# Optimization experiments

Hardware: AMD Instinct MI355X
Metric: run time of the kernel (lower is better)

The kernel has to match this reference:

```python
import jax, jax.numpy as jnp
import numpy as np

N_NODES = 100000
N_EDGES = 1600000
VOCAB = 1000
EMB = 128
HID = 256
N_GRAPHS = 128
N_LABELS = 2


def setup_inputs() -> dict:
    key = jax.random.key(0)
    ks = jax.random.split(key, 16)
    s = 0.05
    inp = {
        "x_ids": jax.random.randint(ks[0], (N_NODES,), 0, VOCAB),
        "edge_index": jax.random.randint(ks[1], (2, N_EDGES), 0, N_NODES),
        "batch": jnp.sort(jax.random.randint(ks[2], (N_NODES,), 0, N_GRAPHS)),
        "emb": jax.random.normal(ks[3], (VOCAB, EMB)) * s,
        "W0": jax.random.normal(ks[4], (EMB, HID)) * s,
        "b0": jnp.zeros((HID,)),
        "W1": jax.random.normal(ks[5], (HID, HID)) * s,
        "b1": jnp.zeros((HID,)),
        "W2": jax.random.normal(ks[6], (HID, HID)) * s,
        "b2": jnp.zeros((HID,)),
        "W3": jax.random.normal(ks[7], (HID, HID)) * s,
        "b3": jnp.zeros((HID,)),
        "Wc1": jax.random.normal(ks[8], (2 * HID, HID)) * s,
        "bc1": jnp.zeros((HID,)),
        "Wc2": jax.random.normal(ks[9], (HID, N_LABELS)) * s,
        "bc2": jnp.zeros((N_LABELS,)),
    }
    return inp


def _gcn_conv(x, W, b, src, dst, dis):
    # GCNConv with self-loops: out = D^-1/2 (A+I) D^-1/2 (x W) + b
    xw = x @ W                                   # [N, H]
    norm = dis[src] * dis[dst]                   # [E]
    out = jnp.zeros_like(xw).at[dst].add(xw[src] * norm[:, None])
    out = out + xw * (dis * dis)[:, None]        # self-loop term
    return out + b


def reference(x_ids, edge_index, batch, emb, W0, b0, W1, b1, W2, b2, W3, b3,
              Wc1, bc1, Wc2, bc2):
    src, dst = edge_index[0], edge_index[1]
    # degree (incl. self loop) is the same every layer -> compute once
    deg = jnp.zeros((N_NODES,), jnp.float32).at[dst].add(1.0) + 1.0
    dis = jax.lax.rsqrt(deg)

    x = emb[x_ids]                               # [N, EMB]
    for W, b in ((W0, b0), (W1, b1), (W2, b2), (W3, b3)):
        x = jax.nn.relu(_gcn_conv(x, W, b, src, dst, dis))
        # dropout: identity in eval mode

    counts = jax.ops.segment_sum(jnp.ones((N_NODES,), x.dtype), batch,
                                 num_segments=N_GRAPHS)
    mean_pool = jax.ops.segment_sum(x, batch, num_segments=N_GRAPHS)
    mean_pool = mean_pool / jnp.maximum(counts, 1.0)[:, None]
    max_pool = jax.ops.segment_max(x, batch, num_segments=N_GRAPHS)
    max_pool = jnp.where(counts[:, None] > 0, max_pool, 0.0)

    g = jnp.concatenate([mean_pool, max_pool], axis=1)  # [G, 2H]
    h = jax.nn.relu(g @ Wc1 + bc1)
    logits = h @ Wc2 + bc2                               # [G, 2]
    return logits
```

## Files before the change

### kernel.cpp

```cpp
#include <hip/hip_runtime.h>
#include <hip/hip_bf16.h>
#include <cstdint>
#include <cstddef>

#define N_NODES 100000
#define N_EDGES 1600000
#define EMBD 128
#define HID 256
#define N_GRAPHS 128
#define VOCAB 1000
#define NB_SCAN 98

typedef short bf16x8 __attribute__((ext_vector_type(8)));
typedef float f32x4 __attribute__((ext_vector_type(4)));
typedef float f32x2 __attribute__((ext_vector_type(2)));

__device__ inline unsigned short rne_bf16(float f) {
  unsigned u = __float_as_uint(f);
  return (unsigned short)((u + 0x7FFFu + ((u >> 16) & 1u)) >> 16);
}
__device__ inline float bf16_to_f32(unsigned short h) {
  return __uint_as_float(((unsigned)h) << 16);
}
__device__ inline void split_hl(float v, unsigned short& h, unsigned short& l) {
  h = rne_bf16(v);
  float hf = __uint_as_float(((unsigned)h) << 16);
  l = rne_bf16(v - hf);
}
__device__ inline f32x4 cvt4(uint2 v) {
  f32x4 r;
  r[0] = __uint_as_float(v.x << 16);
  r[1] = __uint_as_float(v.x & 0xFFFF0000u);
  r[2] = __uint_as_float(v.y << 16);
  r[3] = __uint_as_float(v.y & 0xFFFF0000u);
  return r;
}
__device__ inline f32x2 cvt2(unsigned v) {
  f32x2 r;
  r[0] = __uint_as_float(v << 16);
  r[1] = __uint_as_float(v & 0xFFFF0000u);
  return r;
}

__global__ void k_indeg(const int* __restrict__ dst, int* __restrict__ indeg) {
  int e = blockIdx.x * 256 + threadIdx.x;
  if (e < N_EDGES) atomicAdd(&indeg[dst[e]], 1);
}

__global__ __launch_bounds__(1024)
void k_scan1(const int* __restrict__ indeg, int* __restrict__ off, int* __restrict__ bsum,
             float* __restrict__ dis) {
  __shared__ int s[1024];
  const int tid = threadIdx.x;
  int i = blockIdx.x * 1024 + tid;
  int v = (i < N_NODES) ? indeg[i] : 0;
  if (i < N_NODES) dis[i] = rsqrtf((float)(v + 1));
  s[tid] = v; __syncthreads();
  #pragma unroll
  for (int ofs = 1; ofs < 1024; ofs <<= 1) {
    int t2 = (tid >= ofs) ? s[tid - ofs] : 0;
    __syncthreads();
    s[tid] += t2;
    __syncthreads();
  }
  if (i < N_NODES) off[i] = s[tid] - v;
  if (tid == 1023) bsum[blockIdx.x] = s[1023];
}

__global__ void k_scan2(int* __restrict__ bsum) {
  if (threadIdx.x == 0) {
    int a = 0;
    for (int i = 0; i < NB_SCAN; ++i) { int t = bsum[i]; bsum[i] = a; a += t; }
    bsum[NB_SCAN] = a;
  }
}

__global__ __launch_bounds__(1024)
void k_scan3(int* __restrict__ off, int* __restrict__ cur, const int* __restrict__ bsum) {
  int i = blockIdx.x * 1024 + threadIdx.x;
  if (i < N_NODES) { int v = off[i] + bsum[blockIdx.x]; off[i] = v; cur[i] = v; }
  if (i == 0) off[N_NODES] = bsum[NB_SCAN];
}

__global__ void k_fill(const int* __restrict__ src, const int* __restrict__ dst,
                       const int* __restrict__ ids, const float* __restrict__ dis,
                       int* __restrict__ cursor, int2* __restrict__ csre,
                       int2* __restrict__ csre0) {
  int e = blockIdx.x * 256 + threadIdx.x;
  if (e < N_EDGES) {
    int s = src[e];
    float ds = dis[s];
    int p = atomicAdd(&cursor[dst[e]], 1);
    csre[p]  = make_int2(s, __float_as_int(ds));
    csre0[p] = make_int2(ids[s], __float_as_int(ds));
  }
}

__global__ void k_prep(const float* __restrict__ emb, unsigned short* __restrict__ emb16,
                       const float* __restrict__ W0, unsigned short* __restrict__ w0h,
                       unsigned short* __restrict__ w0l,
                       const float* __restrict__ W1, unsigned short* __restrict__ w1h,
                       unsigned short* __restrict__ w1l,
                       const float* __restrict__ W2, unsigned short* __restrict__ w2h,
                       unsigned short* __restrict__ w2l,
                       const float* __restrict__ W3, unsigned short* __restrict__ w3h,
                       unsigned short* __restrict__ w3l) {
  int i = blockIdx.x * 256 + threadIdx.x;
  if (i < VOCAB * EMBD) { emb16[i] = rne_bf16(emb[i]); return; }
  i -= VOCAB * EMBD;
  unsigned short h, l;
  if (i < EMBD * HID) {
    int k = i >> 8, n = i & 255;
    split_hl(W0[i], h, l);
    w0h[n * EMBD + k] = h; w0l[n * EMBD + k] = l;
    return;
  }
  i -= EMBD * HID;
  if (i >= 3 * HID * HID) return;
  int w = i >> 16, j = i & 65535;
  const float* Ws = (w == 0) ? W1 : (w == 1) ? W2 : W3;
  unsigned short* th = (w == 0) ? w1h : (w == 1) ? w2h : w3h;
  unsigned short* tl = (w == 0) ? w1l : (w == 1) ? w2l : w3l;
  int k = j >> 8, n = j & 255;
  split_hl(Ws[j], h, l);
  th[n * HID + k] = h; tl[n * HID + k] = l;
}

__global__ __launch_bounds__(256)
void k_agg0(const unsigned short* __restrict__ emb16, const int* __restrict__ ids,
            const float* __restrict__ dis, const int* __restrict__ off,
            const int2* __restrict__ csre0, unsigned short* __restrict__ aggA) {
  const int lane = threadIdx.x & 63;
  const int node = blockIdx.x * 4 + (threadIdx.x >> 6);
  const float di = dis[node];
  unsigned sv = *((const unsigned*)(emb16 + (size_t)ids[node] * EMBD) + lane);
  f32x2 a0 = di * cvt2(sv);
  f32x2 a1 = (f32x2)0.f, a2 = (f32x2)0.f, a3 = (f32x2)0.f;
  const int e0 = off[node], e1 = off[node + 1];
  int e = e0;
  for (; e + 4 <= e1; e += 4) {
    int2 c0 = csre0[e], c1 = csre0[e + 1], c2 = csre0[e + 2], c3 = csre0[e + 3];
    unsigned v0 = *((const unsigned*)(emb16 + (size_t)c0.x * EMBD) + lane);
    unsigned v1 = *((const unsigned*)(emb16 + (size_t)c1.x * EMBD) + lane);
    unsigned v2 = *((const unsigned*)(emb16 + (size_t)c2.x * EMBD) + lane);
    unsigned v3 = *((const unsigned*)(emb16 + (size_t)c3.x * EMBD) + lane);
    a0 += __int_as_float(c0.y) * cvt2(v0);
    a1 += __int_as_float(c1.y) * cvt2(v1);
    a2 += __int_as_float(c2.y) * cvt2(v2);
    a3 += __int_as_float(c3.y) * cvt2(v3);
  }
  for (; e < e1; ++e) {
    int2 c0 = csre0[e];
    unsigned v0 = *((const unsigned*)(emb16 + (size_t)c0.x * EMBD) + lane);
    a0 += __int_as_float(c0.y) * cvt2(v0);
  }
  f32x2 r = di * ((a0 + a1) + (a2 + a3));
  size_t base = (size_t)node * EMBD + lane * 2;
  *(ushort2*)&aggA[base] = make_ushort2(rne_bf16(r[0]), rne_bf16(r[1]));
}

__global__ __launch_bounds__(256)
void k_agg16(const unsigned short* __restrict__ y16, const float* __restrict__ dis,
             const int* __restrict__ off, const int2* __restrict__ csre,
             unsigned short* __restrict__ aggA) {
  const int lane = threadIdx.x & 63;
  const int node = blockIdx.x * 4 + (threadIdx.x >> 6);
  const float di = dis[node];
  uint2 sv = *((const uint2*)(y16 + (size_t)node * HID) + lane);
  f32x4 a0 = di * cvt4(sv);
  f32x4 a1 = (f32x4)0.f, a2 = (f32x4)0.f, a3 = (f32x4)0.f;
  const int e0 = off[node], e1 = off[node + 1];
  int e = e0;
  for (; e + 4 <= e1; e += 4) {
    int2 c0 = csre[e], c1 = csre[e + 1], c2 = csre[e + 2], c3 = csre[e + 3];
    uint2 v0 = *((const uint2*)(y16 + (size_t)c0.x * HID) + lane);
    uint2 v1 = *((const uint2*)(y16 + (size_t)c1.x * HID) + lane);
    uint2 v2 = *((const uint2*)(y16 + (size_t)c2.x * HID) + lane);
    uint2 v3 = *((const uint2*)(y16 + (size_t)c3.x * HID) + lane);
    a0 += __int_as_float(c0.y) * cvt4(v0);
    a1 += __int_as_float(c1.y) * cvt4(v1);
    a2 += __int_as_float(c2.y) * cvt4(v2);
    a3 += __int_as_float(c3.y) * cvt4(v3);
  }
  for (; e < e1; ++e) {
    int2 c0 = csre[e];
    uint2 v0 = *((const uint2*)(y16 + (size_t)c0.x * HID) + lane);
    a0 += __int_as_float(c0.y) * cvt4(v0);
  }
  f32x4 r = di * ((a0 + a1) + (a2 + a3));
  size_t base = (size_t)node * HID + lane * 4;
  *(ushort4*)&aggA[base] = make_ushort4(rne_bf16(r[0]), rne_bf16(r[1]),
                                        rne_bf16(r[2]), rne_bf16(r[3]));
}

__device__ inline void gl_lds16(const void* g, void* l) {
  __builtin_amdgcn_global_load_lds((const __attribute__((address_space(1))) unsigned int*)g,
                                   (__attribute__((address_space(3))) unsigned int*)l,
                                   16, 0, 0);
}

template<int K>
__global__ __launch_bounds__(256)
void k_gemm_mfma(const unsigned short* __restrict__ Ah,
                 const unsigned short* __restrict__ Wh, const unsigned short* __restrict__ Wl,
                 const float* __restrict__ bias, unsigned short* __restrict__ C16) {
  __shared__ unsigned short sA[128 * 32];
  __shared__ unsigned short sBh[128 * 32];
  __shared__ unsigned short sBl[128 * 32];
  const int tid = threadIdx.x;
  const int lane = tid & 63;
  const int wid = tid >> 6;
  const int wr = wid >> 1, wc = wid & 1;
  const int row0 = blockIdx.x * 128;
  const int col0 = blockIdx.y * 128;
  const int cl = lane & 15;
  const int sl = lane >> 4;

  f32x4 acc[4][4];
  #pragma unroll
  for (int i = 0; i < 4; ++i)
    #pragma unroll
    for (int j = 0; j < 4; ++j) acc[i][j] = (f32x4)0.f;

  for (int kt = 0; kt < K; kt += 32) {
    #pragma unroll
    for (int q = 0; q < 2; ++q) {
      int c = (wid * 2 + q) * 64 + lane;
      int row = c >> 2, slot = c & 3;
      int ss = slot ^ (row & 3);
      int ga = row0 + row; if (ga > N_NODES - 1) ga = N_NODES - 1;
      size_t aoff = (size_t)ga * K + kt + ss * 8;
      gl_lds16(Ah + aoff, (unsigned short*)sA + (size_t)(wid * 2 + q) * 512);
      size_t boff = (size_t)(col0 + row) * K + kt + ss * 8;
      gl_lds16(Wh + boff, (unsigned short*)sBh + (size_t)(wid * 2 + q) * 512);
      gl_lds16(Wl + boff, (unsigned short*)sBl + (size_t)(wid * 2 + q) * 512);
    }
    __syncthreads();

    bf16x8 fa[4], fbh[4], fbl[4];
    #pragma unroll
    for (int f = 0; f < 4; ++f) {
      int ra = wr * 64 + f * 16 + cl;
      int oa = ra * 32 + ((sl ^ (ra & 3)) << 3);
      fa[f] = *(const bf16x8*)&sA[oa];
      int rb = wc * 64 + f * 16 + cl;
      int ob = rb * 32 + ((sl ^ (rb & 3)) << 3);
      fbh[f] = *(const bf16x8*)&sBh[ob];
      fbl[f] = *(const bf16x8*)&sBl[ob];
    }
    #pragma unroll
    for (int i = 0; i < 4; ++i)
      #pragma unroll
      for (int j = 0; j < 4; ++j) {
        acc[i][j] = __builtin_amdgcn_mfma_f32_16x16x32_bf16(fa[i], fbh[j], acc[i][j], 0, 0, 0);
        acc[i][j] = __builtin_amdgcn_mfma_f32_16x16x32_bf16(fa[i], fbl[j], acc[i][j], 0, 0, 0);
      }
    __syncthreads();
  }

  #pragma unroll
  for (int j = 0; j < 4; ++j) {
    int gn = col0 + wc * 64 + j * 16 + cl;
    float bn = bias[gn];
    #pragma unroll
    for (int i = 0; i < 4; ++i) {
      f32x4 v = acc[i][j];
      #pragma unroll
      for (int r = 0; r < 4; ++r) {
        int gm = row0 + wr * 64 + i * 16 + sl * 4 + r;
        if (gm < N_NODES) C16[(size_t)gm * HID + gn] = rne_bf16(fmaxf(v[r] + bn, 0.f));
      }
    }
  }
}

__device__ inline int lower_bound_i(const int* a, int n, int v) {
  int lo = 0, hi = n;
  while (lo < hi) { int m = (lo + hi) >> 1; if (a[m] < v) lo = m + 1; else hi = m; }
  return lo;
}

__global__ __launch_bounds__(256)
void k_pool(const unsigned short* __restrict__ y16, const int* __restrict__ batch,
            float* __restrict__ g) {
  const int gi = blockIdx.x, t = threadIdx.x;
  const int start = lower_bound_i(batch, N_NODES, gi);
  const int end   = lower_bound_i(batch, N_NODES, gi + 1);
  float sum = 0.f, mx = 0.f;
  #pragma unroll 4
  for (int n = start; n < end; ++n) {
    float v = bf16_to_f32(y16[(size_t)n * HID + t]);
    sum += v; mx = fmaxf(mx, v);
  }
  int cnt = end - start;
  g[gi * 512 + t] = sum / (float)(cnt > 0 ? cnt : 1);
  g[gi * 512 + 256 + t] = mx;
}

__global__ __launch_bounds__(256)
void k_cls(const float* __restrict__ g, const float* __restrict__ Wc1,
           const float* __restrict__ bc1, const float* __restrict__ Wc2,
           const float* __restrict__ bc2, float* __restrict__ out) {
  const int gi = blockIdx.x, t = threadIdx.x;
  __shared__ float sg[512];
  __shared__ float sh[256];
  sg[t] = g[gi * 512 + t];
  sg[256 + t] = g[gi * 512 + 256 + t];
  __syncthreads();
  float a = bc1[t];
  #pragma unroll 8
  for (int k = 0; k < 512; ++k) a = fmaf(sg[k], Wc1[k * HID + t], a);
  sh[t] = fmaxf(a, 0.f);
  __syncthreads();
  if (t < 2) {
    float o = bc2[t];
    for (int k = 0; k < 256; ++k) o = fmaf(sh[k], Wc2[k * 2 + t], o);
    out[gi * 2 + t] = o;
  }
}

extern "C" void kernel_launch(void* const* d_in, const int* in_sizes, int n_in,
                              void* d_out, int out_size, void* d_ws, size_t ws_size,
                              hipStream_t stream) {
  const int*   x_ids = (const int*)d_in[0];
  const int*   ei    = (const int*)d_in[1];
  const int*   batch = (const int*)d_in[2];
  const float* emb   = (const float*)d_in[3];
  const float* W0 = (const float*)d_in[4];  const float* b0 = (const float*)d_in[5];
  const float* W1 = (const float*)d_in[6];  const float* b1 = (const float*)d_in[7];
  const float* W2 = (const float*)d_in[8];  const float* b2 = (const float*)d_in[9];
  const float* W3 = (const float*)d_in[10]; const float* b3 = (const float*)d_in[11];
  const float* Wc1 = (const float*)d_in[12]; const float* bc1 = (const float*)d_in[13];
  const float* Wc2 = (const float*)d_in[14]; const float* bc2 = (const float*)d_in[15];
  float* out = (float*)d_out;
  const int* src = ei;
  const int* dst = ei + N_EDGES;

  char* ws = (char*)d_ws;
  size_t o = 0;
  auto alloc = [&](size_t bytes) -> char* {
    char* p = ws + o; o += (bytes + 255) & ~(size_t)255; return p;
  };
  unsigned short* y16  = (unsigned short*)alloc((size_t)N_NODES * HID * 2);
  unsigned short* aggA = (unsigned short*)alloc((size_t)N_NODES * HID * 2);
  float* dis   = (float*)alloc((size_t)N_NODES * 4);
  int*   indeg = (int*)  alloc((size_t)N_NODES * 4);
  int*   off   = (int*)  alloc((size_t)(N_NODES + 1) * 4);
  int*   cur   = (int*)  alloc((size_t)(N_NODES + 1) * 4);
  int*   bsum  = (int*)  alloc((size_t)(NB_SCAN + 1) * 4);
  int2*  csre  = (int2*) alloc((size_t)N_EDGES * 8);
  int2*  csre0 = (int2*) alloc((size_t)N_EDGES * 8);
  unsigned short* emb16 = (unsigned short*)alloc((size_t)VOCAB * EMBD * 2);
  unsigned short* wbuf  = (unsigned short*)alloc((size_t)458752 * 2);
  float* gf    = (float*)alloc((size_t)N_GRAPHS * 512 * 4);
  (void)ws_size; (void)in_sizes; (void)n_in; (void)out_size;

  unsigned short* wt0h = wbuf;            unsigned short* wt0l = wbuf + 32768;
  unsigned short* wt1h = wbuf + 65536;    unsigned short* wt1l = wbuf + 131072;
  unsigned short* wt2h = wbuf + 196608;   unsigned short* wt2l = wbuf + 262144;
  unsigned short* wt3h = wbuf + 327680;   unsigned short* wt3l = wbuf + 393216;

  hipMemsetAsync(indeg, 0, (size_t)N_NODES * 4, stream);
  k_indeg<<<N_EDGES / 256, 256, 0, stream>>>(dst, indeg);
  k_scan1<<<NB_SCAN, 1024, 0, stream>>>(indeg, off, bsum, dis);
  k_scan2<<<1, 64, 0, stream>>>(bsum);
  k_scan3<<<NB_SCAN, 1024, 0, stream>>>(off, cur, bsum);
  k_fill<<<N_EDGES / 256, 256, 0, stream>>>(src, dst, x_ids, dis, cur, csre, csre0);
  k_prep<<<(VOCAB * EMBD + EMBD * HID + 3 * HID * HID + 255) / 256, 256, 0, stream>>>(
      emb, emb16, W0, wt0h, wt0l, W1, wt1h, wt1l, W2, wt2h, wt2l, W3, wt3h, wt3l);

  dim3 ggrid((N_NODES + 127) / 128, 2);
  k_agg0<<<N_NODES / 4, 256, 0, stream>>>(emb16, x_ids, dis, off, csre0, aggA);
  k_gemm_mfma<128><<<ggrid, 256, 0, stream>>>(aggA, wt0h, wt0l, b0, y16);
  k_agg16<<<N_NODES / 4, 256, 0, stream>>>(y16, dis, off, csre, aggA);
  k_gemm_mfma<256><<<ggrid, 256, 0, stream>>>(aggA, wt1h, wt1l, b1, y16);
  k_agg16<<<N_NODES / 4, 256, 0, stream>>>(y16, dis, off, csre, aggA);
  k_gemm_mfma<256><<<ggrid, 256, 0, stream>>>(aggA, wt2h, wt2l, b2, y16);
  k_agg16<<<N_NODES / 4, 256, 0, stream>>>(y16, dis, off, csre, aggA);
  k_gemm_mfma<256><<<ggrid, 256, 0, stream>>>(aggA, wt3h, wt3l, b3, y16);

  k_pool<<<N_GRAPHS, 256, 0, stream>>>(y16, batch, gf);
  k_cls<<<N_GRAPHS, 256, 0, stream>>>(gf, Wc1, bc1, Wc2, bc2, out);
}
```

Measured before the change: 978.8 us.

## Double-buffer GEMM LDS tiles, unroll aggregation by 8, split pooling across blocks

The MFMA GEMM now uses two LDS buffers per operand, so the next K-tile's global-to-LDS loads are issued before the current tile is consumed. This overlaps load latency with compute, at the cost of twice the shared memory per block, which may lower occupancy. The neighbour aggregation loop is unrolled to 8 edges to keep more gathers in flight. The pooling kernel splits each graph into 4 chunks over a 2D grid and combines results with atomic add/max. The mean division moves into the classifier, and a memset of the accumulators is added so the pooling pass uses more of the GPU.

```diff
diff --git a/kernel.cpp b/kernel.cpp
--- a/kernel.cpp
+++ b/kernel.cpp
@@ -171,6 +171,26 @@
   f32x4 a1 = (f32x4)0.f, a2 = (f32x4)0.f, a3 = (f32x4)0.f;
   const int e0 = off[node], e1 = off[node + 1];
   int e = e0;
+  for (; e + 8 <= e1; e += 8) {
+    int2 c0 = csre[e],     c1 = csre[e + 1], c2 = csre[e + 2], c3 = csre[e + 3];
+    int2 c4 = csre[e + 4], c5 = csre[e + 5], c6 = csre[e + 6], c7 = csre[e + 7];
+    uint2 v0 = *((const uint2*)(y16 + (size_t)c0.x * HID) + lane);
+    uint2 v1 = *((const uint2*)(y16 + (size_t)c1.x * HID) + lane);
+    uint2 v2 = *((const uint2*)(y16 + (size_t)c2.x * HID) + lane);
+    uint2 v3 = *((const uint2*)(y16 + (size_t)c3.x * HID) + lane);
+    uint2 v4 = *((const uint2*)(y16 + (size_t)c4.x * HID) + lane);
+    uint2 v5 = *((const uint2*)(y16 + (size_t)c5.x * HID) + lane);
+    uint2 v6 = *((const uint2*)(y16 + (size_t)c6.x * HID) + lane);
+    uint2 v7 = *((const uint2*)(y16 + (size_t)c7.x * HID) + lane);
+    a0 += __int_as_float(c0.y) * cvt4(v0);
+    a1 += __int_as_float(c1.y) * cvt4(v1);
+    a2 += __int_as_float(c2.y) * cvt4(v2);
+    a3 += __int_as_float(c3.y) * cvt4(v3);
+    a0 += __int_as_float(c4.y) * cvt4(v4);
+    a1 += __int_as_float(c5.y) * cvt4(v5);
+    a2 += __int_as_float(c6.y) * cvt4(v6);
+    a3 += __int_as_float(c7.y) * cvt4(v7);
+  }
   for (; e + 4 <= e1; e += 4) {
     int2 c0 = csre[e], c1 = csre[e + 1], c2 = csre[e + 2], c3 = csre[e + 3];
     uint2 v0 = *((const uint2*)(y16 + (size_t)c0.x * HID) + lane);
@@ -204,9 +224,9 @@
 void k_gemm_mfma(const unsigned short* __restrict__ Ah,
                  const unsigned short* __restrict__ Wh, const unsigned short* __restrict__ Wl,
                  const float* __restrict__ bias, unsigned short* __restrict__ C16) {
-  __shared__ unsigned short sA[128 * 32];
-  __shared__ unsigned short sBh[128 * 32];
-  __shared__ unsigned short sBl[128 * 32];
+  __shared__ unsigned short sA[2][128 * 32];
+  __shared__ unsigned short sBh[2][128 * 32];
+  __shared__ unsigned short sBl[2][128 * 32];
   const int tid = threadIdx.x;
   const int lane = tid & 63;
   const int wid = tid >> 6;
@@ -215,6 +235,7 @@
   const int col0 = blockIdx.y * 128;
   const int cl = lane & 15;
   const int sl = lane >> 4;
+  const int nt = K / 32;
 
   f32x4 acc[4][4];
   #pragma unroll
@@ -222,7 +243,7 @@
     #pragma unroll
     for (int j = 0; j < 4; ++j) acc[i][j] = (f32x4)0.f;
 
-  for (int kt = 0; kt < K; kt += 32) {
+  auto stage = [&](int b, int kt) {
     #pragma unroll
     for (int q = 0; q < 2; ++q) {
       int c = (wid * 2 + q) * 64 + lane;
@@ -230,23 +251,30 @@
       int ss = slot ^ (row & 3);
       int ga = row0 + row; if (ga > N_NODES - 1) ga = N_NODES - 1;
       size_t aoff = (size_t)ga * K + kt + ss * 8;
-      gl_lds16(Ah + aoff, (unsigned short*)sA + (size_t)(wid * 2 + q) * 512);
+      gl_lds16(Ah + aoff, &sA[b][(wid * 2 + q) * 512]);
       size_t boff = (size_t)(col0 + row) * K + kt + ss * 8;
-      gl_lds16(Wh + boff, (unsigned short*)sBh + (size_t)(wid * 2 + q) * 512);
-      gl_lds16(Wl + boff, (unsigned short*)sBl + (size_t)(wid * 2 + q) * 512);
+      gl_lds16(Wh + boff, &sBh[b][(wid * 2 + q) * 512]);
+      gl_lds16(Wl + boff, &sBl[b][(wid * 2 + q) * 512]);
     }
-    __syncthreads();
+  };
+
+  stage(0, 0);
+  __syncthreads();
+
+  for (int t = 0; t < nt; ++t) {
+    const int cur = t & 1;
+    if (t + 1 < nt) stage(cur ^ 1, (t + 1) * 32);
 
     bf16x8 fa[4], fbh[4], fbl[4];
     #pragma unroll
     for (int f = 0; f < 4; ++f) {
       int ra = wr * 64 + f * 16 + cl;
       int oa = ra * 32 + ((sl ^ (ra & 3)) << 3);
-      fa[f] = *(const bf16x8*)&sA[oa];
+      fa[f] = *(const bf16x8*)&sA[cur][oa];
       int rb = wc * 64 + f * 16 + cl;
       int ob = rb * 32 + ((sl ^ (rb & 3)) << 3);
-      fbh[f] = *(const bf16x8*)&sBh[ob];
-      fbl[f] = *(const bf16x8*)&sBl[ob];
+      fbh[f] = *(const bf16x8*)&sBh[cur][ob];
+      fbl[f] = *(const bf16x8*)&sBl[cur][ob];
     }
     #pragma unroll
     for (int i = 0; i < 4; ++i)
@@ -282,30 +310,39 @@
 
 __global__ __launch_bounds__(256)
 void k_pool(const unsigned short* __restrict__ y16, const int* __restrict__ batch,
-            float* __restrict__ g) {
-  const int gi = blockIdx.x, t = threadIdx.x;
+            float* __restrict__ gsum, float* __restrict__ gmax) {
+  const int gi = blockIdx.x, ck = blockIdx.y, t = threadIdx.x;
   const int start = lower_bound_i(batch, N_NODES, gi);
   const int end   = lower_bound_i(batch, N_NODES, gi + 1);
+  const int len = end - start;
+  const int c0 = start + (len * ck) / 4;
+  const int c1 = start + (len * (ck + 1)) / 4;
   float sum = 0.f, mx = 0.f;
   #pragma unroll 4
-  for (int n = start; n < end; ++n) {
+  for (int n = c0; n < c1; ++n) {
     float v = bf16_to_f32(y16[(size_t)n * HID + t]);
     sum += v; mx = fmaxf(mx, v);
   }
-  int cnt = end - start;
-  g[gi * 512 + t] = sum / (float)(cnt > 0 ? cnt : 1);
-  g[gi * 512 + 256 + t] = mx;
+  if (c0 < c1) {
+    atomicAdd(&gsum[gi * HID + t], sum);
+    atomicMax((int*)&gmax[gi * HID + t], __float_as_int(mx));
+  }
 }
 
 __global__ __launch_bounds__(256)
-void k_cls(const float* __restrict__ g, const float* __restrict__ Wc1,
-           const float* __restrict__ bc1, const float* __restrict__ Wc2,
-           const float* __restrict__ bc2, float* __restrict__ out) {
+void k_cls(const float* __restrict__ gsum, const float* __restrict__ gmax,
+           const int* __restrict__ batch,
+           const float* __restrict__ Wc1, const float* __restrict__ bc1,
+           const float* __restrict__ Wc2, const float* __restrict__ bc2,
+           float* __restrict__ out) {
   const int gi = blockIdx.x, t = threadIdx.x;
   __shared__ float sg[512];
   __shared__ float sh[256];
-  sg[t] = g[gi * 512 + t];
-  sg[256 + t] = g[gi * 512 + 256 + t];
+  const int start = lower_bound_i(batch, N_NODES, gi);
+  const int end   = lower_bound_i(batch, N_NODES, gi + 1);
+  const float rcnt = 1.f / (float)((end - start) > 0 ? (end - start) : 1);
+  sg[t] = gsum[gi * HID + t] * rcnt;
+  sg[256 + t] = gmax[gi * HID + t];
   __syncthreads();
   float a = bc1[t];
   #pragma unroll 8
@@ -352,7 +389,8 @@
   int2*  csre0 = (int2*) alloc((size_t)N_EDGES * 8);
   unsigned short* emb16 = (unsigned short*)alloc((size_t)VOCAB * EMBD * 2);
   unsigned short* wbuf  = (unsigned short*)alloc((size_t)458752 * 2);
-  float* gf    = (float*)alloc((size_t)N_GRAPHS * 512 * 4);
+  float* gsum  = (float*)alloc((size_t)N_GRAPHS * HID * 4);
+  float* gmax  = (float*)alloc((size_t)N_GRAPHS * HID * 4);
   (void)ws_size; (void)in_sizes; (void)n_in; (void)out_size;
 
   unsigned short* wt0h = wbuf;            unsigned short* wt0l = wbuf + 32768;
@@ -361,6 +399,7 @@
   unsigned short* wt3h = wbuf + 327680;   unsigned short* wt3l = wbuf + 393216;
 
   hipMemsetAsync(indeg, 0, (size_t)N_NODES * 4, stream);
+  hipMemsetAsync(gsum, 0, (size_t)N_GRAPHS * HID * 4 * 2 + 256, stream);
   k_indeg<<<N_EDGES / 256, 256, 0, stream>>>(dst, indeg);
   k_scan1<<<NB_SCAN, 1024, 0, stream>>>(indeg, off, bsum, dis);
   k_scan2<<<1, 64, 0, stream>>>(bsum);
@@ -379,6 +418,7 @@
   k_agg16<<<N_NODES / 4, 256, 0, stream>>>(y16, dis, off, csre, aggA);
   k_gemm_mfma<256><<<ggrid, 256, 0, stream>>>(aggA, wt3h, wt3l, b3, y16);
 
-  k_pool<<<N_GRAPHS, 256, 0, stream>>>(y16, batch, gf);
-  k_cls<<<N_GRAPHS, 256, 0, stream>>>(gf, Wc1, bc1, Wc2, bc2, out);
-}
+  dim3 pgrid(N_GRAPHS, 4);
+  k_pool<<<pgrid, 256, 0, stream>>>(y16, batch, gsum, gmax);
+  k_cls<<<N_GRAPHS, 256, 0, stream>>>(gsum, gmax, batch, Wc1, bc1, Wc2, bc2, out);
+}
```

Result: faster. 950.6 us (-2.9%).
